# Optimization experiments

Hardware: AMD Instinct MI355X
Metric: run time of the kernel (lower is better)

The kernel has to match this reference:

```python
import jax, jax.numpy as jnp
import numpy as np

N = 1024
H = 4096
W = 4096
K_COUNTS = 10
IOU_T = 0.5
NEG = -1e30  # -inf stand-in for unrecorded groups


def _box_iou(b):
    # b: [N,4] xyxy pixel coords -> [N,N] IoU (torchvision.ops.box_iou)
    area = (b[:, 2] - b[:, 0]) * (b[:, 3] - b[:, 1])
    ix1 = jnp.maximum(b[:, None, 0], b[None, :, 0])
    iy1 = jnp.maximum(b[:, None, 1], b[None, :, 1])
    ix2 = jnp.minimum(b[:, None, 2], b[None, :, 2])
    iy2 = jnp.minimum(b[:, None, 3], b[None, :, 3])
    inter = jnp.clip(ix2 - ix1, 0.0) * jnp.clip(iy2 - iy1, 0.0)
    return inter / (area[:, None] + area[None, :] - inter)


def _c_wsl(iou_gt, scores, counts):
    # Faithful vectorized c_wsl_fast: for every start box i, greedily sweep
    # j = i+1..N-1 adding boxes compatible (IoU <= T) with all current members;
    # when a group hits `counts` at the TOP of a j-iteration it is recorded
    # (check-before-add semantics, so a group completed at j = N-1 is never
    # recorded, matching the original break-based control flow). The final
    # answer is the LAST start achieving the max recorded score (>= update).
    n = scores.shape[0]
    starts = jnp.arange(n)
    carry0 = (
        jnp.eye(n, dtype=bool),            # sel[i, k]: box k in group of start i
        jnp.ones(n, jnp.int32),            # group sizes
        scores,                            # group scores
        jnp.zeros(n, bool),                # recorded flag (== break)
        jnp.full(n, NEG, scores.dtype),    # recorded score
        jnp.zeros((n, n), bool),           # recorded membership
    )

    def step(c, xs):
        j, sj, iou_j = xs  # iou_j = iou_gt[j] (> T bool row; matrix symmetric)
        sel, size, score, rec, rec_score, rec_sel = c
        active = (j > starts) & (~rec)
        do_rec = active & (size == counts)
        rec_sel = jnp.where(do_rec[:, None], sel, rec_sel)
        rec_score = jnp.where(do_rec, score, rec_score)
        rec = rec | do_rec
        compat = ~jnp.any(sel & iou_j[None, :], axis=1)
        add = active & (~do_rec) & (size < counts) & compat
        sel = sel.at[:, j].set(sel[:, j] | add)
        size = size + add.astype(size.dtype)
        score = score + jnp.where(add, sj, jnp.zeros((), score.dtype))
        return (sel, size, score, rec, rec_score, rec_sel), None

    (_, _, _, rec, rec_score, rec_sel), _ = jax.lax.scan(
        step, carry0, (starts, scores, iou_gt))
    masked = jnp.where(rec, rec_score, NEG)
    best = (n - 1) - jnp.argmax(masked[::-1])  # last argmax == '>=' update rule
    return jnp.where(jnp.any(rec), rec_sel[best], jnp.zeros(n, bool))


def reference(bbox, obj_scores, probs, counts):
    Hh, Ww = probs.shape
    # score_bbox_heatmap(reduction='mean'): mean of probs[y1:y2, x1:x2] per box,
    # computed exactly for all boxes with a zero-padded summed-area table.
    sat = jnp.pad(jnp.cumsum(jnp.cumsum(probs, axis=0), axis=1), ((1, 0), (1, 0)))
    x1 = jnp.clip(jnp.floor(bbox[:, 0]).astype(jnp.int32), 0, Ww)
    y1 = jnp.clip(jnp.floor(bbox[:, 1]).astype(jnp.int32), 0, Hh)
    x2 = jnp.clip(jnp.floor(bbox[:, 2]).astype(jnp.int32), 0, Ww)
    y2 = jnp.clip(jnp.floor(bbox[:, 3]).astype(jnp.int32), 0, Hh)
    sums = sat[y2, x2] - sat[y1, x2] - sat[y2, x1] + sat[y1, x1]
    cnt = jnp.maximum((y2 - y1) * (x2 - x1), 1).astype(probs.dtype)
    box_scores = sums / cnt
    # agg_score_method == 'mean'
    scores = 0.5 * (obj_scores + box_scores)
    # sort descending, then greedy IoU grouping on sorted boxes
    order = jnp.argsort(-scores)
    bbox_s = bbox[order]
    scores_s = scores[order]
    iou_gt = _box_iou(bbox_s) > IOU_T
    sel = _c_wsl(iou_gt, scores_s, counts)
    return scores_s * sel.astype(scores_s.dtype)


def setup_inputs() -> dict:
    key = jax.random.key(0)
    k1, k2, k3, k4, k5, k6 = jax.random.split(key, 6)
    cx = jax.random.uniform(k1, (N,), minval=0.15, maxval=0.85) * W
    cy = jax.random.uniform(k2, (N,), minval=0.15, maxval=0.85) * H
    bw = jnp.maximum(jax.random.uniform(k3, (N,), minval=0.02, maxval=0.25) * W, 8.0)
    bh = jnp.maximum(jax.random.uniform(k4, (N,), minval=0.02, maxval=0.25) * H, 8.0)
    bbox = jnp.stack([cx - bw / 2, cy - bh / 2, cx + bw / 2, cy + bh / 2], axis=1)
    obj_scores = jax.random.uniform(k5, (N,))
    probs = jax.random.uniform(k6, (H, W))
    return {"bbox": bbox, "obj_scores": obj_scores, "probs": probs, "counts": K_COUNTS}
```

## Files before the change

### kernel.cpp

```cpp
#include <hip/hip_runtime.h>

#define HH 4096
#define WW 4096
#define NB 1024
#define NCHUNK 256
#define CROWS 16
#define IOU_T 0.5f

typedef unsigned long long u64;

constexpr size_t OFF_PART   = 0;
constexpr size_t OFF_SC64   = OFF_PART   + (size_t)NCHUNK * WW * 8;
constexpr size_t OFF_ORDER  = OFF_SC64   + (size_t)NB * 8;
constexpr size_t OFF_CTR    = OFF_ORDER  + (size_t)NB * 4;
constexpr size_t OFF_IOU    = OFF_CTR    + 64;
constexpr size_t OFF_RECSC  = OFF_IOU    + (size_t)NB * 16 * 8;
constexpr size_t OFF_RECSEL = OFF_RECSC  + (size_t)NB * 8;
constexpr size_t OFF_CC     = OFF_RECSEL + (size_t)NB * 16 * 8;


__global__ void __launch_bounds__(256) k_stage(const float* __restrict__ probs,
        const float* __restrict__ bbox,
        double* __restrict__ part, float* __restrict__ Cc) {
    __shared__ int xlo_s[CROWS], xhi_s[CROWS];
    __shared__ int2 rng_s[CROWS];
    int tid = blockIdx.x * 256 + threadIdx.x;
    int c  = tid >> 10;
    int xq = tid & 1023;
    int t  = threadIdx.x;
    if (t < CROWS) { xlo_s[t] = WW + 1; xhi_s[t] = -1; }
    __syncthreads();
    int r0 = c * CROWS;
    for (int i = t; i < NB; i += 256) {
        float4 bb = ((const float4*)bbox)[i];
        int x1 = min(max((int)floorf(bb.x), 0), WW);
        int y1 = min(max((int)floorf(bb.y), 0), HH);
        int x2 = min(max((int)floorf(bb.z), 0), WW);
        int y2 = min(max((int)floorf(bb.w), 0), HH);
        int ra = y1 - 1 - r0, rb = y2 - 1 - r0;
        if (ra >= 0 && ra < CROWS) { atomicMin(&xlo_s[ra], x1); atomicMax(&xhi_s[ra], x2); }
        if (rb >= 0 && rb < CROWS) { atomicMin(&xlo_s[rb], x1); atomicMax(&xhi_s[rb], x2); }
    }
    __syncthreads();
    if (t < CROWS) {
        int lo = xlo_s[t], hi = xhi_s[t];
        rng_s[t] = (hi >= 0) ? make_int2(lo >> 2, (hi + 3) >> 2) : make_int2(1, 0);
    }
    __syncthreads();
    const float4* p = (const float4*)probs + (size_t)r0 * (WW / 4) + xq;
    float4* Cc4 = (float4*)Cc;
    double a0 = 0.0, a1 = 0.0, a2 = 0.0, a3 = 0.0;
    for (int r = 0; r < CROWS; r += 8) {
        float4 q[8];
        #pragma unroll
        for (int k = 0; k < 8; k++) q[k] = p[(size_t)(r + k) * (WW / 4)];
        #pragma unroll
        for (int k = 0; k < 8; k++) {
            a0 += (double)q[k].x; a1 += (double)q[k].y;
            a2 += (double)q[k].z; a3 += (double)q[k].w;
            int2 d = rng_s[r + k];
            if (xq >= d.x && xq < d.y)
                Cc4[(size_t)(r0 + r + k) * (WW / 4) + xq] =
                    make_float4((float)a0, (float)a1, (float)a2, (float)a3);
        }
    }
    double2* pp = (double2*)(part + (size_t)c * WW) + xq * 2;
    pp[0] = make_double2(a0, a1);
    pp[1] = make_double2(a2, a3);
}

__global__ void __launch_bounds__(256) k_chunkscan(double* __restrict__ part,
                                                   int* __restrict__ ctr) {
    if (blockIdx.x == 0 && threadIdx.x == 0) *ctr = 0;
    __shared__ double wsum[4];
    int col = blockIdx.x;
    int t = threadIdx.x;
    int lane = t & 63, wv = t >> 6;
    double v = part[(size_t)t * WW + col];
    double inc = v;
    #pragma unroll
    for (int off = 1; off < 64; off <<= 1) {
        double n = __shfl_up(inc, off);
        if (lane >= off) inc += n;
    }
    if (lane == 63) wsum[wv] = inc;
    __syncthreads();
    double woff = 0.0;
    for (int w = 0; w < 3; w++) if (w < wv) woff += wsum[w];
    part[(size_t)t * WW + col] = woff + (inc - v);
}

__global__ void __launch_bounds__(256) k_boxsum(const float* __restrict__ bbox,
                         const float* __restrict__ obj,
                         const float* __restrict__ Cc,
                         const double* __restrict__ part,
                         double* __restrict__ sc64) {
    int i = blockIdx.x;
    int t = threadIdx.x;
    float4 bb = ((const float4*)bbox)[i];
    int x1 = min(max((int)floorf(bb.x), 0), WW);
    int y1 = min(max((int)floorf(bb.y), 0), HH);
    int x2 = min(max((int)floorf(bb.z), 0), WW);
    int y2 = min(max((int)floorf(bb.w), 0), HH);
    bool h1 = (y1 >= 1), h2 = (y2 >= 1);
    const float*  r2 = Cc   + (size_t)(h2 ? (y2 - 1) : 0) * WW;
    const double* q2 = part + (size_t)(h2 ? ((y2 - 1) >> 4) : 0) * WW;
    const float*  r1 = Cc   + (size_t)(h1 ? (y1 - 1) : 0) * WW;
    const double* q1 = part + (size_t)(h1 ? ((y1 - 1) >> 4) : 0) * WW;
    double s = 0.0;
    for (int x = x1 + t; x < x2; x += 256) {
        double v2 = h2 ? ((double)r2[x] + q2[x]) : 0.0;
        double v1 = h1 ? ((double)r1[x] + q1[x]) : 0.0;
        s += (v2 - v1);
    }
    __shared__ double red[4];
    #pragma unroll
    for (int off = 32; off > 0; off >>= 1) s += __shfl_down(s, off);
    if ((t & 63) == 0) red[t >> 6] = s;
    __syncthreads();
    if (t == 0) {
        double tot = red[0] + red[1] + red[2] + red[3];
        long long cnt = (long long)(y2 - y1) * (long long)(x2 - x1);
        if (cnt < 1) cnt = 1;
        sc64[i] = 0.5 * ((double)obj[i] + tot / (double)cnt);
    }
}

__global__ void __launch_bounds__(128) k_rank(const double* __restrict__ sc64,
                                              int* __restrict__ order) {
    __shared__ double s[NB];
    int t = threadIdx.x;
    for (int k = t; k < NB; k += 128) s[k] = sc64[k];
    __syncthreads();
    int i = blockIdx.x * 128 + t;
    double si = s[i];
    int rank = 0;
    #pragma unroll 8
    for (int j = 0; j < NB; j++) {
        double sj = s[j];
        rank += (sj > si) || (sj == si && j < i);
    }
    order[rank] = i;
}

__global__ void k_iou(const int* __restrict__ order, const float* __restrict__ bbox,
                      u64* __restrict__ ioub) {
    int tid = blockIdx.x * blockDim.x + threadIdx.x;
    int i = tid >> 10;
    int j = tid & (NB - 1);
    float4 a = ((const float4*)bbox)[order[i]];
    float4 b = ((const float4*)bbox)[order[j]];
    float ai = (a.z - a.x) * (a.w - a.y);
    float aj = (b.z - b.x) * (b.w - b.y);
    float ix1 = fmaxf(a.x, b.x), iy1 = fmaxf(a.y, b.y);
    float ix2 = fminf(a.z, b.z), iy2 = fminf(a.w, b.w);
    float iw = fmaxf(ix2 - ix1, 0.0f), ih = fmaxf(iy2 - iy1, 0.0f);
    float inter = iw * ih;
    float iou_v = inter / (ai + aj - inter);
    bool bit = iou_v > IOU_T;
    u64 m = __ballot(bit);
    if ((threadIdx.x & 63) == 0) ioub[(size_t)i * 16 + (j >> 6)] = m;
}

__global__ void __launch_bounds__(64) k_group(const u64* __restrict__ ioub,
                        const int* __restrict__ order,
                        const double* __restrict__ sc64,
                        const int* __restrict__ counts,
                        double* __restrict__ recsc,
                        u64* __restrict__ recsel,
                        int* __restrict__ ctr,
                        float* __restrict__ out) {
    __shared__ double ssd_s[NB];
    __shared__ int lastflag;
    int t = threadIdx.x;
    int i = blockIdx.x * 64 + t;
    for (int k = t; k < NB; k += 64) ssd_s[k] = sc64[order[k]];
    __syncthreads();
    int K = counts[0];
    u64 inc[16], sel[16];
    int wi = i >> 6, bi = i & 63;
    #pragma unroll
    for (int w = 0; w < 16; w++) {
        inc[w] = ioub[(size_t)i * 16 + w];
        sel[w] = (w == wi) ? (1ULL << bi) : 0ULL;
    }
    int size = 1;
    double score = ssd_s[i];
    int last = i;
    #pragma unroll
    for (int w = 0; w < 16; w++) {
        if (w < wi || size >= K) continue;
        u64 avail = ~inc[w];
        if (w == wi) avail &= (bi == 63) ? 0ULL : (~0ULL << (bi + 1));
        while (avail != 0ULL && size < K) {
            int b = __builtin_ctzll(avail);
            int j = (w << 6) + b;
            sel[w] |= 1ULL << b;
            size++;
            score += ssd_s[j];
            last = j;
            const u64* rj = ioub + (size_t)j * 16;
            #pragma unroll
            for (int w2 = 0; w2 < 16; w2++) inc[w2] |= rj[w2];
            avail &= ~inc[w];
            avail &= ~(1ULL << b);
        }
    }
    int rec = (size == K) && (last < NB - 1);
    recsc[i] = rec ? score : -1e300;
    #pragma unroll
    for (int w = 0; w < 16; w++) recsel[(size_t)i * 16 + w] = sel[w];
    __threadfence();
    if (t == 0) lastflag = (atomicAdd(ctr, 1) == (int)gridDim.x - 1);
    __syncthreads();
    if (!lastflag) return;
    __threadfence();
    double bs = -1e301; int bidx = 0;
    for (int m = 0; m < 16; m++) {
        int k = t * 16 + m;
        double v = recsc[k];
        if (v >= bs) { bs = v; bidx = k; }
    }
    #pragma unroll
    for (int off = 32; off > 0; off >>= 1) {
        double ob = __shfl_down(bs, off);
        int oi = __shfl_down(bidx, off);
        if (ob > bs || (ob == bs && oi > bidx)) { bs = ob; bidx = oi; }
    }
    bs = __shfl(bs, 0);
    bidx = __shfl(bidx, 0);
    int any = bs > -1e299;
    for (int k = t; k < NB; k += 64) {
        float v = 0.0f;
        if (any && ((recsel[(size_t)bidx * 16 + (k >> 6)] >> (k & 63)) & 1ULL))
            v = (float)ssd_s[k];
        out[k] = v;
    }
}


extern "C" void kernel_launch(void* const* d_in, const int* in_sizes, int n_in,
                              void* d_out, int out_size, void* d_ws, size_t ws_size,
                              hipStream_t stream) {
    const float* bbox  = (const float*)d_in[0];
    const float* obj   = (const float*)d_in[1];
    const float* probs = (const float*)d_in[2];
    const int*   counts = (const int*)d_in[3];
    float* out = (float*)d_out;

    char* w = (char*)d_ws;
    double* part    = (double*)(w + OFF_PART);
    double* sc64    = (double*)(w + OFF_SC64);
    int*    order   = (int*)(w + OFF_ORDER);
    int*    ctr     = (int*)(w + OFF_CTR);
    u64*    ioub    = (u64*)(w + OFF_IOU);
    double* recsc   = (double*)(w + OFF_RECSC);
    u64*    recsel  = (u64*)(w + OFF_RECSEL);
    float*  Cc      = (float*)(w + OFF_CC);

    k_stage<<<(NCHUNK * WW / 4) / 256, 256, 0, stream>>>(probs, bbox, part, Cc);
    k_chunkscan<<<WW, 256, 0, stream>>>(part, ctr);
    k_boxsum<<<NB, 256, 0, stream>>>(bbox, obj, Cc, part, sc64);
    k_rank<<<NB / 128, 128, 0, stream>>>(sc64, order);
    k_iou<<<(NB * NB) / 256, 256, 0, stream>>>(order, bbox, ioub);
    k_group<<<NB / 64, 64, 0, stream>>>(ioub, order, sc64, counts, recsc, recsel,
                                        ctr, out);
}
```

Before: 186.2 us.

## Fuse rank, IoU and grouping into one persistent kernel; coarsen scan chunks

Replaces the separate rank, IoU-bitmask and grouping kernels with a single 32-block kernel that uses atomic grid barriers between phases, removing two kernel launches and their gaps. The row-chunk size for the two-level prefix sum grows from 16 to 64 rows, so there are fewer chunk partials. The chunk scan becomes a per-column serial loop over 64 chunks instead of a block-wide shuffle scan. The grid barrier depends on all 32 blocks being co-resident, and the fused kernel runs the IoU and rank phases on far fewer threads. k_stage now runs 64-row serial accumulation per thread with fewer blocks, which may reduce parallelism in the heavy streaming pass.

```diff
diff --git a/kernel.cpp b/kernel.cpp
--- a/kernel.cpp
+++ b/kernel.cpp
@@ -3,17 +3,18 @@
 #define HH 4096
 #define WW 4096
 #define NB 1024
-#define NCHUNK 256
-#define CROWS 16
+#define NCHUNK 64
+#define CROWS 64
 #define IOU_T 0.5f
+#define FBLK 32
 
 typedef unsigned long long u64;
 
 constexpr size_t OFF_PART   = 0;
 constexpr size_t OFF_SC64   = OFF_PART   + (size_t)NCHUNK * WW * 8;
 constexpr size_t OFF_ORDER  = OFF_SC64   + (size_t)NB * 8;
-constexpr size_t OFF_CTR    = OFF_ORDER  + (size_t)NB * 4;
-constexpr size_t OFF_IOU    = OFF_CTR    + 64;
+constexpr size_t OFF_BAR    = OFF_ORDER  + (size_t)NB * 4;
+constexpr size_t OFF_IOU    = OFF_BAR    + 64;
 constexpr size_t OFF_RECSC  = OFF_IOU    + (size_t)NB * 16 * 8;
 constexpr size_t OFF_RECSEL = OFF_RECSC  + (size_t)NB * 8;
 constexpr size_t OFF_CC     = OFF_RECSEL + (size_t)NB * 16 * 8;
@@ -21,13 +22,14 @@
 
 __global__ void __launch_bounds__(256) k_stage(const float* __restrict__ probs,
         const float* __restrict__ bbox,
-        double* __restrict__ part, float* __restrict__ Cc) {
+        double* __restrict__ part, float* __restrict__ Cc, int* __restrict__ bar) {
     __shared__ int xlo_s[CROWS], xhi_s[CROWS];
     __shared__ int2 rng_s[CROWS];
     int tid = blockIdx.x * 256 + threadIdx.x;
     int c  = tid >> 10;
     int xq = tid & 1023;
     int t  = threadIdx.x;
+    if (blockIdx.x == 0 && t < 16) bar[t] = 0;
     if (t < CROWS) { xlo_s[t] = WW + 1; xhi_s[t] = -1; }
     __syncthreads();
     int r0 = c * CROWS;
@@ -69,25 +71,18 @@
     pp[1] = make_double2(a2, a3);
 }
 
-__global__ void __launch_bounds__(256) k_chunkscan(double* __restrict__ part,
-                                                   int* __restrict__ ctr) {
-    if (blockIdx.x == 0 && threadIdx.x == 0) *ctr = 0;
-    __shared__ double wsum[4];
-    int col = blockIdx.x;
-    int t = threadIdx.x;
-    int lane = t & 63, wv = t >> 6;
-    double v = part[(size_t)t * WW + col];
-    double inc = v;
-    #pragma unroll
-    for (int off = 1; off < 64; off <<= 1) {
-        double n = __shfl_up(inc, off);
-        if (lane >= off) inc += n;
-    }
-    if (lane == 63) wsum[wv] = inc;
-    __syncthreads();
-    double woff = 0.0;
-    for (int w = 0; w < 3; w++) if (w < wv) woff += wsum[w];
-    part[(size_t)t * WW + col] = woff + (inc - v);
+__global__ void k_chunkscan(double* __restrict__ part) {
+    int x = blockIdx.x * blockDim.x + threadIdx.x;
+    double carry = 0.0;
+    for (int g = 0; g < NCHUNK / 16; g++) {
+        double v[16];
+        #pragma unroll
+        for (int k = 0; k < 16; k++) v[k] = part[(size_t)(g * 16 + k) * WW + x];
+        #pragma unroll
+        for (int k = 0; k < 16; k++) { double tv = v[k]; v[k] = carry; carry += tv; }
+        #pragma unroll
+        for (int k = 0; k < 16; k++) part[(size_t)(g * 16 + k) * WW + x] = v[k];
+    }
 }
 
 __global__ void __launch_bounds__(256) k_boxsum(const float* __restrict__ bbox,
@@ -104,9 +99,9 @@
     int y2 = min(max((int)floorf(bb.w), 0), HH);
     bool h1 = (y1 >= 1), h2 = (y2 >= 1);
     const float*  r2 = Cc   + (size_t)(h2 ? (y2 - 1) : 0) * WW;
-    const double* q2 = part + (size_t)(h2 ? ((y2 - 1) >> 4) : 0) * WW;
+    const double* q2 = part + (size_t)(h2 ? ((y2 - 1) >> 6) : 0) * WW;
     const float*  r1 = Cc   + (size_t)(h1 ? (y1 - 1) : 0) * WW;
-    const double* q1 = part + (size_t)(h1 ? ((y1 - 1) >> 4) : 0) * WW;
+    const double* q1 = part + (size_t)(h1 ? ((y1 - 1) >> 6) : 0) * WW;
     double s = 0.0;
     for (int x = x1 + t; x < x2; x += 256) {
         double v2 = h2 ? ((double)r2[x] + q2[x]) : 0.0;
@@ -126,114 +121,148 @@
     }
 }
 
-__global__ void __launch_bounds__(128) k_rank(const double* __restrict__ sc64,
-                                              int* __restrict__ order) {
-    __shared__ double s[NB];
-    int t = threadIdx.x;
-    for (int k = t; k < NB; k += 128) s[k] = sc64[k];
-    __syncthreads();
-    int i = blockIdx.x * 128 + t;
-    double si = s[i];
-    int rank = 0;
-    #pragma unroll 8
-    for (int j = 0; j < NB; j++) {
-        double sj = s[j];
-        rank += (sj > si) || (sj == si && j < i);
-    }
-    order[rank] = i;
-}
-
-__global__ void k_iou(const int* __restrict__ order, const float* __restrict__ bbox,
-                      u64* __restrict__ ioub) {
-    int tid = blockIdx.x * blockDim.x + threadIdx.x;
-    int i = tid >> 10;
-    int j = tid & (NB - 1);
-    float4 a = ((const float4*)bbox)[order[i]];
-    float4 b = ((const float4*)bbox)[order[j]];
-    float ai = (a.z - a.x) * (a.w - a.y);
-    float aj = (b.z - b.x) * (b.w - b.y);
-    float ix1 = fmaxf(a.x, b.x), iy1 = fmaxf(a.y, b.y);
-    float ix2 = fminf(a.z, b.z), iy2 = fminf(a.w, b.w);
-    float iw = fmaxf(ix2 - ix1, 0.0f), ih = fmaxf(iy2 - iy1, 0.0f);
-    float inter = iw * ih;
-    float iou_v = inter / (ai + aj - inter);
-    bool bit = iou_v > IOU_T;
-    u64 m = __ballot(bit);
-    if ((threadIdx.x & 63) == 0) ioub[(size_t)i * 16 + (j >> 6)] = m;
-}
-
-__global__ void __launch_bounds__(64) k_group(const u64* __restrict__ ioub,
-                        const int* __restrict__ order,
+__device__ __forceinline__ void gridbar(int* bar, int slot) {
+    __syncthreads();
+    if (threadIdx.x == 0) {
+        __threadfence();
+        atomicAdd(&bar[slot], 1);
+        while (atomicAdd(&bar[slot], 0) < FBLK) {}
+        __threadfence();
+    }
+    __syncthreads();
+}
+
+__global__ void __launch_bounds__(256) k_fused(const float* __restrict__ bbox,
                         const double* __restrict__ sc64,
                         const int* __restrict__ counts,
+                        int* __restrict__ order,
+                        u64* __restrict__ ioub,
                         double* __restrict__ recsc,
                         u64* __restrict__ recsel,
-                        int* __restrict__ ctr,
+                        int* __restrict__ bar,
                         float* __restrict__ out) {
-    __shared__ double ssd_s[NB];
-    __shared__ int lastflag;
-    int t = threadIdx.x;
-    int i = blockIdx.x * 64 + t;
-    for (int k = t; k < NB; k += 64) ssd_s[k] = sc64[order[k]];
-    __syncthreads();
-    int K = counts[0];
-    u64 inc[16], sel[16];
-    int wi = i >> 6, bi = i & 63;
-    #pragma unroll
-    for (int w = 0; w < 16; w++) {
-        inc[w] = ioub[(size_t)i * 16 + w];
-        sel[w] = (w == wi) ? (1ULL << bi) : 0ULL;
-    }
-    int size = 1;
-    double score = ssd_s[i];
-    int last = i;
-    #pragma unroll
-    for (int w = 0; w < 16; w++) {
-        if (w < wi || size >= K) continue;
-        u64 avail = ~inc[w];
-        if (w == wi) avail &= (bi == 63) ? 0ULL : (~0ULL << (bi + 1));
-        while (avail != 0ULL && size < K) {
-            int b = __builtin_ctzll(avail);
-            int j = (w << 6) + b;
-            sel[w] |= 1ULL << b;
-            size++;
-            score += ssd_s[j];
-            last = j;
-            const u64* rj = ioub + (size_t)j * 16;
+    __shared__ double s[NB];
+    __shared__ int rnk[256];
+    int t = threadIdx.x, b = blockIdx.x;
+    for (int k = t; k < NB; k += 256) s[k] = sc64[k];
+    __syncthreads();
+    {
+        int il = t >> 3;
+        int i = b * 32 + il;
+        int jp = t & 7;
+        double si = s[i];
+        int rank = 0;
+        int j0 = jp * 128;
+        #pragma unroll 8
+        for (int j = j0; j < j0 + 128; j++) {
+            double sj = s[j];
+            rank += (sj > si) || (sj == si && j < i);
+        }
+        rnk[t] = rank;
+        __syncthreads();
+        if (jp == 0) {
+            int r = 0;
             #pragma unroll
-            for (int w2 = 0; w2 < 16; w2++) inc[w2] |= rj[w2];
-            avail &= ~inc[w];
-            avail &= ~(1ULL << b);
-        }
-    }
-    int rec = (size == K) && (last < NB - 1);
-    recsc[i] = rec ? score : -1e300;
-    #pragma unroll
-    for (int w = 0; w < 16; w++) recsel[(size_t)i * 16 + w] = sel[w];
-    __threadfence();
-    if (t == 0) lastflag = (atomicAdd(ctr, 1) == (int)gridDim.x - 1);
-    __syncthreads();
-    if (!lastflag) return;
-    __threadfence();
-    double bs = -1e301; int bidx = 0;
-    for (int m = 0; m < 16; m++) {
-        int k = t * 16 + m;
+            for (int k = 0; k < 8; k++) r += rnk[(il << 3) + k];
+            order[r] = i;
+        }
+    }
+    gridbar(bar, 0);
+    for (int k = t; k < NB; k += 256) s[k] = sc64[order[k]];
+    {
+        int wv = (b * 256 + t) >> 6;
+        int lane = t & 63;
+        for (int w = wv; w < NB * 16; w += FBLK * 4) {
+            int i = w >> 4;
+            int j = ((w & 15) << 6) + lane;
+            float4 a = ((const float4*)bbox)[order[i]];
+            float4 bb = ((const float4*)bbox)[order[j]];
+            float ai = (a.z - a.x) * (a.w - a.y);
+            float aj = (bb.z - bb.x) * (bb.w - bb.y);
+            float ix1 = fmaxf(a.x, bb.x), iy1 = fmaxf(a.y, bb.y);
+            float ix2 = fminf(a.z, bb.z), iy2 = fminf(a.w, bb.w);
+            float iw = fmaxf(ix2 - ix1, 0.0f), ih = fmaxf(iy2 - iy1, 0.0f);
+            float inter = iw * ih;
+            float iou_v = inter / (ai + aj - inter);
+            u64 m = __ballot(iou_v > IOU_T);
+            if (lane == 0) ioub[w] = m;
+        }
+    }
+    gridbar(bar, 1);
+    if (t < 32) {
+        int i = b * 32 + t;
+        int K = counts[0];
+        u64 inc[16], sel[16];
+        int wi = i >> 6, bi = i & 63;
+        #pragma unroll
+        for (int w = 0; w < 16; w++) {
+            inc[w] = ioub[(size_t)i * 16 + w];
+            sel[w] = (w == wi) ? (1ULL << bi) : 0ULL;
+        }
+        int size = 1;
+        double score = s[i];
+        int last = i;
+        #pragma unroll
+        for (int w = 0; w < 16; w++) {
+            if (w < wi || size >= K) continue;
+            u64 avail = ~inc[w];
+            if (w == wi) avail &= (bi == 63) ? 0ULL : (~0ULL << (bi + 1));
+            while (avail != 0ULL && size < K) {
+                int bb = __builtin_ctzll(avail);
+                int j = (w << 6) + bb;
+                sel[w] |= 1ULL << bb;
+                size++;
+                score += s[j];
+                last = j;
+                const u64* rj = ioub + (size_t)j * 16;
+                #pragma unroll
+                for (int w2 = 0; w2 < 16; w2++) inc[w2] |= rj[w2];
+                avail &= ~inc[w];
+                avail &= ~(1ULL << bb);
+            }
+        }
+        int rec = (size == K) && (last < NB - 1);
+        recsc[i] = rec ? score : -1e300;
+        #pragma unroll
+        for (int w = 0; w < 16; w++) recsel[(size_t)i * 16 + w] = sel[w];
+    }
+    __syncthreads();
+    if (t == 0) {
+        __threadfence();
+        atomicAdd(&bar[2], 1);
+    }
+    if (b != 0) return;
+    if (t == 0) {
+        while (atomicAdd(&bar[2], 0) < FBLK) {}
+        __threadfence();
+    }
+    __syncthreads();
+    __shared__ double bsc[256];
+    __shared__ int bidx[256];
+    double bs = -1e301; int bi = 0;
+    for (int m = 0; m < 4; m++) {
+        int k = t * 4 + m;
         double v = recsc[k];
-        if (v >= bs) { bs = v; bidx = k; }
-    }
-    #pragma unroll
-    for (int off = 32; off > 0; off >>= 1) {
-        double ob = __shfl_down(bs, off);
-        int oi = __shfl_down(bidx, off);
-        if (ob > bs || (ob == bs && oi > bidx)) { bs = ob; bidx = oi; }
-    }
-    bs = __shfl(bs, 0);
-    bidx = __shfl(bidx, 0);
-    int any = bs > -1e299;
-    for (int k = t; k < NB; k += 64) {
+        if (v >= bs) { bs = v; bi = k; }
+    }
+    bsc[t] = bs; bidx[t] = bi;
+    __syncthreads();
+    for (int st = 128; st > 0; st >>= 1) {
+        if (t < st) {
+            if (bsc[t + st] > bsc[t] ||
+                (bsc[t + st] == bsc[t] && bidx[t + st] > bidx[t])) {
+                bsc[t] = bsc[t + st];
+                bidx[t] = bidx[t + st];
+            }
+        }
+        __syncthreads();
+    }
+    int best = bidx[0];
+    int any = bsc[0] > -1e299;
+    for (int k = t; k < NB; k += 256) {
         float v = 0.0f;
-        if (any && ((recsel[(size_t)bidx * 16 + (k >> 6)] >> (k & 63)) & 1ULL))
-            v = (float)ssd_s[k];
+        if (any && ((recsel[(size_t)best * 16 + (k >> 6)] >> (k & 63)) & 1ULL))
+            v = (float)s[k];
         out[k] = v;
     }
 }
@@ -252,17 +281,15 @@
     double* part    = (double*)(w + OFF_PART);
     double* sc64    = (double*)(w + OFF_SC64);
     int*    order   = (int*)(w + OFF_ORDER);
-    int*    ctr     = (int*)(w + OFF_CTR);
+    int*    bar     = (int*)(w + OFF_BAR);
     u64*    ioub    = (u64*)(w + OFF_IOU);
     double* recsc   = (double*)(w + OFF_RECSC);
     u64*    recsel  = (u64*)(w + OFF_RECSEL);
     float*  Cc      = (float*)(w + OFF_CC);
 
-    k_stage<<<(NCHUNK * WW / 4) / 256, 256, 0, stream>>>(probs, bbox, part, Cc);
-    k_chunkscan<<<WW, 256, 0, stream>>>(part, ctr);
+    k_stage<<<(NCHUNK * WW / 4) / 256, 256, 0, stream>>>(probs, bbox, part, Cc, bar);
+    k_chunkscan<<<WW / 256, 256, 0, stream>>>(part);
     k_boxsum<<<NB, 256, 0, stream>>>(bbox, obj, Cc, part, sc64);
-    k_rank<<<NB / 128, 128, 0, stream>>>(sc64, order);
-    k_iou<<<(NB * NB) / 256, 256, 0, stream>>>(order, bbox, ioub);
-    k_group<<<NB / 64, 64, 0, stream>>>(ioub, order, sc64, counts, recsc, recsel,
-                                        ctr, out);
-}
+    k_fused<<<FBLK, 256, 0, stream>>>(bbox, sc64, counts, order, ioub,
+                                      recsc, recsel, bar, out);
+}
```

New measurement: 178.4 us. 1.04x faster.
